# Optimization experiments

Measured on AMD Instinct MI355X. Metric: run time of the kernel, lower is better.

The kernel has to match this reference:

```python
import jax, jax.numpy as jnp
import numpy as np
from jax import ops as jops

N_NODES = 50000
N_EDGES = 800000
IN_CH = 128
HIDDEN = 32
HEADS = 8
OUT_CH = 128
NUM_GRAPHS = 64


def setup_inputs() -> dict:
    key = jax.random.key(0)
    ks = jax.random.split(key, 12)
    x = jax.random.normal(ks[0], (N_NODES, IN_CH), dtype=jnp.float32)
    edge_index = jax.random.randint(ks[1], (2, N_EDGES), 0, N_NODES, dtype=jnp.int64)
    batch = jnp.sort(jax.random.randint(ks[2], (N_NODES,), 0, NUM_GRAPHS, dtype=jnp.int64))
    HC = HEADS * HIDDEN  # 256
    s = lambda fan: 1.0 / np.sqrt(fan)
    W_gat = jax.random.normal(ks[3], (IN_CH, HC), dtype=jnp.float32) * s(IN_CH)
    att_src = jax.random.normal(ks[4], (HEADS, HIDDEN), dtype=jnp.float32) * s(HIDDEN)
    att_dst = jax.random.normal(ks[5], (HEADS, HIDDEN), dtype=jnp.float32) * s(HIDDEN)
    b_gat = jnp.zeros((HC,), dtype=jnp.float32)
    W1 = jax.random.normal(ks[6], (HC, HIDDEN), dtype=jnp.float32) * s(HC)
    b1 = jnp.zeros((HIDDEN,), dtype=jnp.float32)
    W2 = jax.random.normal(ks[7], (HIDDEN, HIDDEN), dtype=jnp.float32) * s(HIDDEN)
    b2 = jnp.zeros((HIDDEN,), dtype=jnp.float32)
    Wf = jax.random.normal(ks[8], (HIDDEN, OUT_CH), dtype=jnp.float32) * s(HIDDEN)
    bf = jnp.zeros((OUT_CH,), dtype=jnp.float32)
    return {"x": x, "edge_index": edge_index, "batch": batch,
            "W_gat": W_gat, "att_src": att_src, "att_dst": att_dst, "b_gat": b_gat,
            "W1": W1, "b1": b1, "W2": W2, "b2": b2, "Wf": Wf, "bf": bf}


def _gat(x, src, dst, N, W_gat, att_src, att_dst, b_gat):
    # h: [N, H, C]
    h = (x @ W_gat).reshape(N, HEADS, HIDDEN)
    a_s = jnp.sum(h * att_src[None], axis=-1)  # [N, H]
    a_d = jnp.sum(h * att_dst[None], axis=-1)  # [N, H]
    e = jax.nn.leaky_relu(a_s[src] + a_d[dst], negative_slope=0.2)  # [E, H]
    # per-destination-node softmax over incoming edges
    m = jops.segment_max(e, dst, num_segments=N)          # [N, H]
    ex = jnp.exp(e - m[dst])                              # [E, H]
    denom = jops.segment_sum(ex, dst, num_segments=N)     # [N, H]
    alpha = ex / denom[dst]                               # [E, H]
    msg = alpha[:, :, None] * h[src]                      # [E, H, C]
    out = jops.segment_sum(msg, dst, num_segments=N)      # [N, H, C]
    return out.reshape(N, HEADS * HIDDEN) + b_gat


def reference(x, edge_index, batch, W_gat, att_src, att_dst, b_gat,
              W1, b1, W2, b2, Wf, bf):
    N = x.shape[0]
    # GATConv (PyG default add_self_loops=True)
    loops = jnp.arange(N, dtype=edge_index.dtype)
    src = jnp.concatenate([edge_index[0], loops])
    dst = jnp.concatenate([edge_index[1], loops])
    out = jax.nn.relu(_gat(x, src, dst, N, W_gat, att_src, att_dst, b_gat))
    # GINConv (eps=0, no self-loops): nn((1+eps)*x + sum_{j->i} x_j)
    agg = jops.segment_sum(out[edge_index[0]], edge_index[1], num_segments=N)
    z = out + agg
    z = jax.nn.relu(z @ W1 + b1) @ W2 + b2
    z = jax.nn.relu(z)
    # global mean pool over graphs
    sums = jops.segment_sum(z, batch, num_segments=NUM_GRAPHS)
    counts = jops.segment_sum(jnp.ones((N,), dtype=z.dtype), batch, num_segments=NUM_GRAPHS)
    pooled = sums / jnp.maximum(counts, 1.0)[:, None]
    return pooled @ Wf + bf
```

## Files before the change

kernel.cpp:

```cpp
#include <hip/hip_runtime.h>

#define N_NODES 50000
#define N_EDGES 800000
#define HEADS   8
#define HID     32
#define HC      256
#define NG      64
#define GEMM_TILES (N_NODES / 16)
#define NBUCK   196
#define EBUF_CAP 5120
#define BUCKA_BLOCKS 196

typedef unsigned short ushort_t;
typedef unsigned int   uint_t;
typedef __attribute__((ext_vector_type(8))) short short8;
typedef __attribute__((ext_vector_type(4))) float f32x4;

#define HB_OFF    0
#define Z_OFF     0
#define AS_OFF    6400000
#define AD_OFF    6800000
#define ROW_OFF   7200000
#define BCNT_OFF  7250016
#define BBASE_OFF 7256288
#define GS_OFF    7256544
#define WGBT_OFF  7256640
#define W1BT_OFF  7273024
#define CSR_OFF   7277120
#define EBUF_OFF  8077120
#define Y_OFF     10084160
#define WS_END    10884160

__device__ __forceinline__ ushort_t f2bf(float f) {
    uint_t u = __float_as_uint(f);
    u = (u + 0x7FFFu + ((u >> 16) & 1u)) >> 16;
    return (ushort_t)u;
}
__device__ __forceinline__ float bf2f(ushort_t u) { return __uint_as_float((uint_t)u << 16); }
__device__ __forceinline__ float bf_lo(uint_t u) { return __uint_as_float(u << 16); }
__device__ __forceinline__ float bf_hi(uint_t u) { return __uint_as_float(u & 0xFFFF0000u); }

__global__ __launch_bounds__(256) void k_init(const float* __restrict__ Wg,
                                              const float* __restrict__ W1,
                                              ushort_t* __restrict__ wgbT,
                                              ushort_t* __restrict__ w1bT,
                                              float* __restrict__ bcntf) {
    int id = blockIdx.x * 256 + threadIdx.x;
    if (id < 32768) {
        wgbT[(id & 255) * 128 + (id >> 8)] = f2bf(Wg[id]);
    } else if (id < 32768 + 1568) {
        ((float4*)bcntf)[id - 32768] = make_float4(0.f, 0.f, 0.f, 0.f);
    } else if (id < 32768 + 1568 + 8192) {
        int j = id - 32768 - 1568;
        w1bT[(j & 31) * 256 + (j >> 5)] = f2bf(W1[j]);
    }
}

__global__ __launch_bounds__(256) void k_gemm_bucketA(const float* __restrict__ x,
                                                      const ushort_t* __restrict__ wgbT,
                                                      const float* __restrict__ att_s,
                                                      const float* __restrict__ att_d,
                                                      ushort_t* __restrict__ hb,
                                                      float* __restrict__ a_s,
                                                      float* __restrict__ a_d,
                                                      const int* __restrict__ batch,
                                                      int* __restrict__ gs,
                                                      const int* __restrict__ ei,
                                                      int* __restrict__ bcnt,
                                                      int* __restrict__ ebuf) {
    if (blockIdx.x < BUCKA_BLOCKS) {
        __shared__ int h[NBUCK];
        __shared__ int base[NBUCK];
        int kb = blockIdx.x;
        int t = threadIdx.x;
        if (t < NBUCK) h[t] = 0;
        __syncthreads();
        int pack[16];
#pragma unroll
        for (int i = 0; i < 16; ++i) {
            int e = kb * 4096 + i * 256 + t;
            pack[i] = -1;
            if (e < N_EDGES) {
                int b = ei[N_EDGES + e] >> 8;
                int lp = atomicAdd(&h[b], 1);
                pack[i] = (b << 16) | lp;
            }
        }
        __syncthreads();
        if (t < NBUCK && h[t] > 0) base[t] = atomicAdd(&bcnt[t * 32], h[t]);
        __syncthreads();
        int2* eb = (int2*)ebuf;
#pragma unroll
        for (int i = 0; i < 16; ++i) {
            if (pack[i] >= 0) {
                int e = kb * 4096 + i * 256 + t;
                int b = pack[i] >> 16, lp = pack[i] & 0xFFFF;
                eb[(size_t)b * EBUF_CAP + base[b] + lp] = make_int2(ei[e], ei[N_EDGES + e]);
            }
        }
        return;
    }

    int tile = blockIdx.x - BUCKA_BLOCKS;
    int w = threadIdx.x >> 6;
    int colbase = w * 64;
    int lane = threadIdx.x & 63;
    int n0 = tile * 16;
    int col = lane & 15, quad = lane >> 4;

    f32x4 acc[4];
#pragma unroll
    for (int i = 0; i < 4; ++i) acc[i] = (f32x4){0.f, 0.f, 0.f, 0.f};

    const float* xr = x + (size_t)(n0 + col) * 128 + quad * 8;
    const ushort_t* wbase = wgbT + (size_t)(colbase + col) * 128 + quad * 8;
#pragma unroll
    for (int kk = 0; kk < 4; ++kk) {
        float4 xa = *(const float4*)(xr + kk * 32);
        float4 xb = *(const float4*)(xr + kk * 32 + 4);
        short8 af;
        af[0] = (short)f2bf(xa.x); af[1] = (short)f2bf(xa.y);
        af[2] = (short)f2bf(xa.z); af[3] = (short)f2bf(xa.w);
        af[4] = (short)f2bf(xb.x); af[5] = (short)f2bf(xb.y);
        af[6] = (short)f2bf(xb.z); af[7] = (short)f2bf(xb.w);
#pragma unroll
        for (int nt = 0; nt < 4; ++nt) {
            short8 wf = *(const short8*)(wbase + nt * 16 * 128 + kk * 32);
            acc[nt] = __builtin_amdgcn_mfma_f32_16x16x32_bf16(wf, af, acc[nt], 0, 0, 0);
        }
    }

    int node = n0 + col;
    ushort_t* hrow = hb + (size_t)node * 256 + colbase + quad * 4;
#pragma unroll
    for (int nt = 0; nt < 4; ++nt) {
        uint2 o;
        o.x = (uint_t)f2bf(acc[nt][0]) | ((uint_t)f2bf(acc[nt][1]) << 16);
        o.y = (uint_t)f2bf(acc[nt][2]) | ((uint_t)f2bf(acc[nt][3]) << 16);
        *(uint2*)(hrow + nt * 16) = o;
    }

#pragma unroll
    for (int hl = 0; hl < 2; ++hl) {
        int hg = (colbase >> 5) + hl;
        float4 s0 = *(const float4*)(att_s + colbase + hl * 32 + quad * 4);
        float4 s1 = *(const float4*)(att_s + colbase + hl * 32 + 16 + quad * 4);
        float4 d0 = *(const float4*)(att_d + colbase + hl * 32 + quad * 4);
        float4 d1 = *(const float4*)(att_d + colbase + hl * 32 + 16 + quad * 4);
        f32x4 e = acc[2 * hl], f = acc[2 * hl + 1];
        float ps = e[0]*s0.x + e[1]*s0.y + e[2]*s0.z + e[3]*s0.w
                 + f[0]*s1.x + f[1]*s1.y + f[2]*s1.z + f[3]*s1.w;
        float pd = e[0]*d0.x + e[1]*d0.y + e[2]*d0.z + e[3]*d0.w
                 + f[0]*d1.x + f[1]*d1.y + f[2]*d1.z + f[3]*d1.w;
        ps += __shfl_xor(ps, 16, 64); ps += __shfl_xor(ps, 32, 64);
        pd += __shfl_xor(pd, 16, 64); pd += __shfl_xor(pd, 32, 64);
        if (quad == 0) {
            a_s[(size_t)node * 8 + hg] = ps;
            a_d[(size_t)node * 8 + hg] = pd;
        }
    }

    int t = threadIdx.x;
    if (t < 16) {
        int n = n0 + t;
        int b0 = batch[n];
        int bp = (n == 0) ? -1 : batch[n - 1];
        for (int g2 = bp + 1; g2 <= b0; ++g2) gs[g2] = n;
        if (n == N_NODES - 1)
            for (int g2 = b0 + 1; g2 <= NG; ++g2) gs[g2] = N_NODES;
    }
}

__global__ __launch_bounds__(512) void k_bucketB(const int* __restrict__ ebuf,
                                                 const int* __restrict__ bcnt,
                                                 int* __restrict__ row,
                                                 int* __restrict__ csr) {
    __shared__ int h[256], sc[256], cur[256];
    int k = blockIdx.x, t = threadIdx.x;
    if (t < 256) sc[t] = (t < NBUCK) ? bcnt[t * 32] : 0;
    __syncthreads();
    for (int off = 1; off < 256; off <<= 1) {
        int u = 0;
        if (t < 256 && t >= off) u = sc[t - off];
        __syncthreads();
        if (t < 256) sc[t] += u;
        __syncthreads();
    }
    int base = (k == 0) ? 0 : sc[k - 1];
    int cnt = bcnt[k * 32];
    __syncthreads();
    if (t < 256) { h[t] = 0; cur[t] = 0; }
    __syncthreads();
    const int2* eb = (const int2*)ebuf + (size_t)k * EBUF_CAP;
    for (int i = t; i < cnt; i += 512) atomicAdd(&h[eb[i].y & 255], 1);
    __syncthreads();
    int v = (t < 256) ? h[t] : 0;
    if (t < 256) sc[t] = v;
    __syncthreads();
    for (int off = 1; off < 256; off <<= 1) {
        int u = 0;
        if (t < 256 && t >= off) u = sc[t - off];
        __syncthreads();
        if (t < 256) sc[t] += u;
        __syncthreads();
    }
    int lrow = 0;
    if (t < 256) {
        lrow = sc[t] - v;
        int n = k * 256 + t;
        if (n < N_NODES) row[n] = base + lrow;
    }
    if (k == 0 && t == 0) row[N_NODES] = N_EDGES;
    __syncthreads();
    if (t < 256) sc[t] = lrow;
    __syncthreads();
    for (int i = t; i < cnt; i += 512) {
        int2 sd = eb[i];
        int dl = sd.y & 255;
        int p = atomicAdd(&cur[dl], 1);
        csr[base + sc[dl] + p] = sd.x;
    }
}

__global__ __launch_bounds__(256) void k_gat_y(const int* __restrict__ row,
                                               const int* __restrict__ csr,
                                               const float* __restrict__ a_s,
                                               const float* __restrict__ a_d,
                                               const ushort_t* __restrict__ hb,
                                               const float* __restrict__ bg,
                                               const ushort_t* __restrict__ w1bT,
                                               ushort_t* __restrict__ yb) {
    __shared__ ushort_t s_out[16][264];
    int w = threadIdx.x >> 6;
    int lane = threadIdx.x & 63;
    int n0 = blockIdx.x * 16;

    int c    = lane & 31;
    int half = lane >> 5;
    int hd   = c >> 2;
    const char* as_hd = (const char*)(a_s + hd);
    const char* hlane = (const char*)hb + c * 16;
    float4 b0 = *(const float4*)(bg + c * 8);
    float4 b1 = *(const float4*)(bg + c * 8 + 4);

    for (int i = 0; i < 4; ++i) {
        int n = n0 + w * 4 + i;
        int r0 = row[n], r1 = row[n + 1];
        int deg = r1 - r0;
        float ad2 = a_d[n * 8 + hd];
        const int* cp = csr + r0;

        float acc[8];
        float psum;
        {
            float vs = *(const float*)(as_hd + ((size_t)n << 5)) + ad2;
            vs = vs > 0.f ? vs : 0.2f * vs;
            float evs = __expf(vs);
            float wq = (half == 0) ? evs : 0.f;
            uint4 su = *(const uint4*)(hlane + ((size_t)n << 9));
            acc[0] = wq * bf_lo(su.x); acc[1] = wq * bf_hi(su.x);
            acc[2] = wq * bf_lo(su.y); acc[3] = wq * bf_hi(su.y);
            acc[4] = wq * bf_lo(su.z); acc[5] = wq * bf_hi(su.z);
            acc[6] = wq * bf_lo(su.w); acc[7] = wq * bf_hi(su.w);
            psum = wq;
        }

        int j = half;
        for (; j + 6 < deg; j += 8) {
            int   sx[4];
            float av[4];
            uint4 uu[4];
#pragma unroll
            for (int q = 0; q < 4; ++q) sx[q] = cp[j + 2 * q];
#pragma unroll
            for (int q = 0; q < 4; ++q) av[q] = *(const float*)(as_hd + ((size_t)sx[q] << 5));
#pragma unroll
            for (int q = 0; q < 4; ++q) uu[q] = *(const uint4*)(hlane + ((size_t)sx[q] << 9));
#pragma unroll
            for (int q = 0; q < 4; ++q) {
                float v = av[q] + ad2;
                v = v > 0.f ? v : 0.2f * v;
                float ev = __expf(v);
                psum += ev;
                acc[0] = fmaf(ev, bf_lo(uu[q].x), acc[0]);
                acc[1] = fmaf(ev, bf_hi(uu[q].x), acc[1]);
                acc[2] = fmaf(ev, bf_lo(uu[q].y), acc[2]);
                acc[3] = fmaf(ev, bf_hi(uu[q].y), acc[3]);
                acc[4] = fmaf(ev, bf_lo(uu[q].z), acc[4]);
                acc[5] = fmaf(ev, bf_hi(uu[q].z), acc[5]);
                acc[6] = fmaf(ev, bf_lo(uu[q].w), acc[6]);
                acc[7] = fmaf(ev, bf_hi(uu[q].w), acc[7]);
            }
        }
        for (; j < deg; j += 2) {
            int sj = cp[j];
            float v = *(const float*)(as_hd + ((size_t)sj << 5)) + ad2;
            v = v > 0.f ? v : 0.2f * v;
            float ev = __expf(v);
            psum += ev;
            uint4 u = *(const uint4*)(hlane + ((size_t)sj << 9));
            acc[0] = fmaf(ev, bf_lo(u.x), acc[0]);
            acc[1] = fmaf(ev, bf_hi(u.x), acc[1]);
            acc[2] = fmaf(ev, bf_lo(u.y), acc[2]);
            acc[3] = fmaf(ev, bf_hi(u.y), acc[3]);
            acc[4] = fmaf(ev, bf_lo(u.z), acc[4]);
            acc[5] = fmaf(ev, bf_hi(u.z), acc[5]);
            acc[6] = fmaf(ev, bf_lo(u.w), acc[6]);
            acc[7] = fmaf(ev, bf_hi(u.w), acc[7]);
        }

        psum += __shfl_xor(psum, 32, 64);
#pragma unroll
        for (int k2 = 0; k2 < 8; ++k2) acc[k2] += __shfl_xor(acc[k2], 32, 64);

        float inv = 1.0f / psum;
        float o0 = fmaxf(fmaf(acc[0], inv, b0.x), 0.f);
        float o1 = fmaxf(fmaf(acc[1], inv, b0.y), 0.f);
        float o2 = fmaxf(fmaf(acc[2], inv, b0.z), 0.f);
        float o3 = fmaxf(fmaf(acc[3], inv, b0.w), 0.f);
        float o4 = fmaxf(fmaf(acc[4], inv, b1.x), 0.f);
        float o5 = fmaxf(fmaf(acc[5], inv, b1.y), 0.f);
        float o6 = fmaxf(fmaf(acc[6], inv, b1.z), 0.f);
        float o7 = fmaxf(fmaf(acc[7], inv, b1.w), 0.f);
        uint4 o;
        o.x = (uint_t)f2bf(o0) | ((uint_t)f2bf(o1) << 16);
        o.y = (uint_t)f2bf(o2) | ((uint_t)f2bf(o3) << 16);
        o.z = (uint_t)f2bf(o4) | ((uint_t)f2bf(o5) << 16);
        o.w = (uint_t)f2bf(o6) | ((uint_t)f2bf(o7) << 16);
        if (half == 0)
            *(uint4*)&s_out[w * 4 + i][c * 8] = o;
    }
    __syncthreads();

    if (w < 2) {
        int col = lane & 15, quad = lane >> 4;
        f32x4 acc = (f32x4){0.f, 0.f, 0.f, 0.f};
        const ushort_t* ar = &s_out[col][quad * 8];
        const ushort_t* bp = w1bT + (w * 16 + col) * 256 + quad * 8;
#pragma unroll
        for (int kk = 0; kk < 8; ++kk) {
            short8 af = *(const short8*)(ar + kk * 32);
            short8 bf0 = *(const short8*)(bp + kk * 32);
            acc = __builtin_amdgcn_mfma_f32_16x16x32_bf16(af, bf0, acc, 0, 0, 0);
        }
        ushort_t* yr = yb + (size_t)(n0 + quad * 4) * 32 + w * 16 + col;
#pragma unroll
        for (int r = 0; r < 4; ++r)
            yr[r * 32] = f2bf(acc[r]);
    }
}

__global__ __launch_bounds__(256) void k_gin_mlp(const int* __restrict__ row,
                                                 const int* __restrict__ csr,
                                                 const ushort_t* __restrict__ yb,
                                                 const float* __restrict__ b1,
                                                 const float* __restrict__ W2,
                                                 const float* __restrict__ b2,
                                                 float* __restrict__ z) {
    __shared__ float s_z[4][32];
    int g = threadIdx.x >> 6;
    int lane = threadIdx.x & 63;
    int n = blockIdx.x * 4 + g;
    int col = lane & 31, half = lane >> 5;
    int r0 = row[n], r1 = row[n + 1];
    const char* ycol = (const char*)(yb + col);
    float acc = (half == 0) ? (bf2f(yb[(size_t)n * 32 + col]) + b1[col]) : 0.f;
    int j = r0 + half;
    for (; j + 14 < r1; j += 16) {
        int ss[8];
#pragma unroll
        for (int i = 0; i < 8; ++i) ss[i] = csr[j + 2 * i];
        float vv[8];
#pragma unroll
        for (int i = 0; i < 8; ++i)
            vv[i] = bf2f(*(const ushort_t*)(ycol + ((size_t)ss[i] << 6)));
        acc += ((vv[0] + vv[1]) + (vv[2] + vv[3])) + ((vv[4] + vv[5]) + (vv[6] + vv[7]));
    }
    for (; j + 6 < r1; j += 8) {
        int s0 = csr[j], s1 = csr[j + 2], s2 = csr[j + 4], s3 = csr[j + 6];
        float v0 = bf2f(*(const ushort_t*)(ycol + ((size_t)s0 << 6)));
        float v1 = bf2f(*(const ushort_t*)(ycol + ((size_t)s1 << 6)));
        float v2 = bf2f(*(const ushort_t*)(ycol + ((size_t)s2 << 6)));
        float v3 = bf2f(*(const ushort_t*)(ycol + ((size_t)s3 << 6)));
        acc += (v0 + v1) + (v2 + v3);
    }
    for (; j < r1; j += 2)
        acc += bf2f(*(const ushort_t*)(ycol + ((size_t)csr[j] << 6)));
    acc += __shfl_xor(acc, 32, 64);
    float z1 = fmaxf(acc, 0.f);
    if (lane < 32) s_z[g][col] = z1;
    const float* zr = &s_z[g][0];
    int k0 = half * 16;
    float p = 0.f;
#pragma unroll
    for (int k = 0; k < 16; k += 4) {
        float4 zv = *(const float4*)(zr + k0 + k);
        p = fmaf(zv.x, W2[(k0 + k + 0) * 32 + col], p);
        p = fmaf(zv.y, W2[(k0 + k + 1) * 32 + col], p);
        p = fmaf(zv.z, W2[(k0 + k + 2) * 32 + col], p);
        p = fmaf(zv.w, W2[(k0 + k + 3) * 32 + col], p);
    }
    p += __shfl_xor(p, 32, 64);
    if (lane < 32) z[n * 32 + col] = fmaxf(p + b2[col], 0.f);
}

__global__ __launch_bounds__(128) void k_pool_final(const float* __restrict__ z,
                                                    const int* __restrict__ gs,
                                                    const float* __restrict__ Wf,
                                                    const float* __restrict__ bf,
                                                    float* __restrict__ outp) {
    __shared__ float part[4][32];
    __shared__ float sums[32];
    int g = blockIdx.x;
    int t = threadIdx.x;
    int col = t & 31, q = t >> 5;
    int r0 = gs[g], r1 = gs[g + 1];
    float s = 0.f;
    for (int r = r0 + q; r < r1; r += 4) s += z[r * 32 + col];
    part[q][col] = s;
    __syncthreads();
    if (t < 32) sums[t] = part[0][t] + part[1][t] + part[2][t] + part[3][t];
    __syncthreads();
    float inv = 1.0f / fmaxf((float)(r1 - r0), 1.0f);
    float acc = 0.f;
#pragma unroll
    for (int k = 0; k < 32; ++k)
        acc = fmaf(sums[k], Wf[k * 128 + t], acc);
    outp[g * 128 + t] = acc * inv + bf[t];
}

extern "C" void kernel_launch(void* const* d_in, const int* in_sizes, int n_in,
                              void* d_out, int out_size, void* d_ws, size_t ws_size,
                              hipStream_t stream) {
    const float* x     = (const float*)d_in[0];
    const int*   ei    = (const int*)d_in[1];
    const int*   batch = (const int*)d_in[2];
    const float* Wg    = (const float*)d_in[3];
    const float* att_s = (const float*)d_in[4];
    const float* att_d = (const float*)d_in[5];
    const float* bg    = (const float*)d_in[6];
    const float* W1    = (const float*)d_in[7];
    const float* b1    = (const float*)d_in[8];
    const float* W2    = (const float*)d_in[9];
    const float* b2    = (const float*)d_in[10];
    const float* Wf    = (const float*)d_in[11];
    const float* bf    = (const float*)d_in[12];
    float* ws = (float*)d_ws;

    ushort_t* hb   = (ushort_t*)(ws + HB_OFF);
    float* z       = ws + Z_OFF;
    float* a_s     = ws + AS_OFF;
    float* a_d     = ws + AD_OFF;
    int*   row     = (int*)(ws + ROW_OFF);
    int*   bcnt    = (int*)(ws + BCNT_OFF);
    int*   gs      = (int*)(ws + GS_OFF);
    ushort_t* wgbT = (ushort_t*)(ws + WGBT_OFF);
    ushort_t* w1bT = (ushort_t*)(ws + W1BT_OFF);
    int*   csr     = (int*)(ws + CSR_OFF);
    int*   ebuf    = (int*)(ws + EBUF_OFF);
    ushort_t* yb   = (ushort_t*)(ws + Y_OFF);

    k_init<<<(32768 + 1568 + 8192 + 255) / 256, 256, 0, stream>>>(Wg, W1, wgbT, w1bT, (float*)bcnt);

    k_gemm_bucketA<<<BUCKA_BLOCKS + GEMM_TILES, 256, 0, stream>>>(
        x, wgbT, att_s, att_d, hb, a_s, a_d, batch, gs, ei, bcnt, ebuf);

    k_bucketB<<<NBUCK, 512, 0, stream>>>(ebuf, bcnt, row, csr);

    k_gat_y<<<N_NODES / 16, 256, 0, stream>>>(row, csr, a_s, a_d, hb, bg, w1bT, yb);

    k_gin_mlp<<<N_NODES / 4, 256, 0, stream>>>(row, csr, yb, b1, W2, b2, z);

    k_pool_final<<<NG, 128, 0, stream>>>(z, gs, Wf, bf, (float*)d_out);
}
```

Before: 301.8 us.

## Regroup pipeline kernels: fuse weight init with bucketA, bucketB with GAT GEMM

Measured after the change: 309.7 us. 1.03x slower.

```diff
diff --git a/kernel.cpp b/kernel.cpp
--- a/kernel.cpp
+++ b/kernel.cpp
@@ -10,6 +10,7 @@
 #define NBUCK   196
 #define EBUF_CAP 5120
 #define BUCKA_BLOCKS 196
+#define INIT_BLOCKS 160
 
 typedef unsigned short ushort_t;
 typedef unsigned int   uint_t;
@@ -40,23 +41,59 @@
 __device__ __forceinline__ float bf_lo(uint_t u) { return __uint_as_float(u << 16); }
 __device__ __forceinline__ float bf_hi(uint_t u) { return __uint_as_float(u & 0xFFFF0000u); }
 
-__global__ __launch_bounds__(256) void k_init(const float* __restrict__ Wg,
-                                              const float* __restrict__ W1,
-                                              ushort_t* __restrict__ wgbT,
-                                              ushort_t* __restrict__ w1bT,
-                                              float* __restrict__ bcntf) {
-    int id = blockIdx.x * 256 + threadIdx.x;
-    if (id < 32768) {
-        wgbT[(id & 255) * 128 + (id >> 8)] = f2bf(Wg[id]);
-    } else if (id < 32768 + 1568) {
-        ((float4*)bcntf)[id - 32768] = make_float4(0.f, 0.f, 0.f, 0.f);
-    } else if (id < 32768 + 1568 + 8192) {
-        int j = id - 32768 - 1568;
-        w1bT[(j & 31) * 256 + (j >> 5)] = f2bf(W1[j]);
-    }
-}
-
-__global__ __launch_bounds__(256) void k_gemm_bucketA(const float* __restrict__ x,
+__global__ __launch_bounds__(256) void k_init_bucketA(const float* __restrict__ Wg,
+                                                      const float* __restrict__ W1,
+                                                      ushort_t* __restrict__ wgbT,
+                                                      ushort_t* __restrict__ w1bT,
+                                                      const int* __restrict__ ei,
+                                                      int* __restrict__ bcnt,
+                                                      int* __restrict__ ebuf) {
+    if (blockIdx.x < INIT_BLOCKS) {
+        int id = blockIdx.x * 256 + threadIdx.x;
+        if (id < 32768) {
+            wgbT[(id & 255) * 128 + (id >> 8)] = f2bf(Wg[id]);
+        } else {
+            int j = id - 32768;
+            w1bT[(j & 31) * 256 + (j >> 5)] = f2bf(W1[j]);
+        }
+        return;
+    }
+    __shared__ int h[NBUCK];
+    __shared__ int base[NBUCK];
+    int kb = blockIdx.x - INIT_BLOCKS;
+    int t = threadIdx.x;
+    if (t < NBUCK) h[t] = 0;
+    __syncthreads();
+    int pack[16];
+#pragma unroll
+    for (int i = 0; i < 16; ++i) {
+        int e = kb * 4096 + i * 256 + t;
+        pack[i] = -1;
+        if (e < N_EDGES) {
+            int b = ei[N_EDGES + e] >> 8;
+            int lp = atomicAdd(&h[b], 1);
+            pack[i] = (b << 16) | lp;
+        }
+    }
+    __syncthreads();
+    if (t < NBUCK && h[t] > 0) base[t] = atomicAdd(&bcnt[t * 32], h[t]);
+    __syncthreads();
+    int2* eb = (int2*)ebuf;
+#pragma unroll
+    for (int i = 0; i < 16; ++i) {
+        if (pack[i] >= 0) {
+            int e = kb * 4096 + i * 256 + t;
+            int b = pack[i] >> 16, lp = pack[i] & 0xFFFF;
+            eb[(size_t)b * EBUF_CAP + base[b] + lp] = make_int2(ei[e], ei[N_EDGES + e]);
+        }
+    }
+}
+
+__global__ __launch_bounds__(256) void k_bucketB_gemm(const int* __restrict__ ebuf,
+                                                      const int* __restrict__ bcnt,
+                                                      int* __restrict__ row,
+                                                      int* __restrict__ csr,
+                                                      const float* __restrict__ x,
                                                       const ushort_t* __restrict__ wgbT,
                                                       const float* __restrict__ att_s,
                                                       const float* __restrict__ att_d,
@@ -64,44 +101,52 @@
                                                       float* __restrict__ a_s,
                                                       float* __restrict__ a_d,
                                                       const int* __restrict__ batch,
-                                                      int* __restrict__ gs,
-                                                      const int* __restrict__ ei,
-                                                      int* __restrict__ bcnt,
-                                                      int* __restrict__ ebuf) {
-    if (blockIdx.x < BUCKA_BLOCKS) {
-        __shared__ int h[NBUCK];
-        __shared__ int base[NBUCK];
-        int kb = blockIdx.x;
-        int t = threadIdx.x;
-        if (t < NBUCK) h[t] = 0;
-        __syncthreads();
-        int pack[16];
-#pragma unroll
-        for (int i = 0; i < 16; ++i) {
-            int e = kb * 4096 + i * 256 + t;
-            pack[i] = -1;
-            if (e < N_EDGES) {
-                int b = ei[N_EDGES + e] >> 8;
-                int lp = atomicAdd(&h[b], 1);
-                pack[i] = (b << 16) | lp;
-            }
-        }
-        __syncthreads();
-        if (t < NBUCK && h[t] > 0) base[t] = atomicAdd(&bcnt[t * 32], h[t]);
-        __syncthreads();
-        int2* eb = (int2*)ebuf;
-#pragma unroll
-        for (int i = 0; i < 16; ++i) {
-            if (pack[i] >= 0) {
-                int e = kb * 4096 + i * 256 + t;
-                int b = pack[i] >> 16, lp = pack[i] & 0xFFFF;
-                eb[(size_t)b * EBUF_CAP + base[b] + lp] = make_int2(ei[e], ei[N_EDGES + e]);
-            }
+                                                      int* __restrict__ gs) {
+    if (blockIdx.x < NBUCK) {
+        __shared__ int h[256], sc[256], cur[256];
+        int k = blockIdx.x, t = threadIdx.x;
+        sc[t] = (t < NBUCK) ? bcnt[t * 32] : 0;
+        __syncthreads();
+        for (int off = 1; off < 256; off <<= 1) {
+            int u = (t >= off) ? sc[t - off] : 0;
+            __syncthreads();
+            sc[t] += u;
+            __syncthreads();
+        }
+        int base = (k == 0) ? 0 : sc[k - 1];
+        int cnt = bcnt[k * 32];
+        __syncthreads();
+        h[t] = 0; cur[t] = 0;
+        __syncthreads();
+        const int2* eb = (const int2*)ebuf + (size_t)k * EBUF_CAP;
+        for (int i = t; i < cnt; i += 256) atomicAdd(&h[eb[i].y & 255], 1);
+        __syncthreads();
+        int v = h[t];
+        sc[t] = v;
+        __syncthreads();
+        for (int off = 1; off < 256; off <<= 1) {
+            int u = (t >= off) ? sc[t - off] : 0;
+            __syncthreads();
+            sc[t] += u;
+            __syncthreads();
+        }
+        int lrow = sc[t] - v;
+        int n = k * 256 + t;
+        if (n < N_NODES) row[n] = base + lrow;
+        if (k == 0 && t == 0) row[N_NODES] = N_EDGES;
+        __syncthreads();
+        sc[t] = lrow;
+        __syncthreads();
+        for (int i = t; i < cnt; i += 256) {
+            int2 sd = eb[i];
+            int dl = sd.y & 255;
+            int p = atomicAdd(&cur[dl], 1);
+            csr[base + sc[dl] + p] = sd.x;
         }
         return;
     }
 
-    int tile = blockIdx.x - BUCKA_BLOCKS;
+    int tile = blockIdx.x - NBUCK;
     int w = threadIdx.x >> 6;
     int colbase = w * 64;
     int lane = threadIdx.x & 63;
@@ -171,57 +216,6 @@
     }
 }
 
-__global__ __launch_bounds__(512) void k_bucketB(const int* __restrict__ ebuf,
-                                                 const int* __restrict__ bcnt,
-                                                 int* __restrict__ row,
-                                                 int* __restrict__ csr) {
-    __shared__ int h[256], sc[256], cur[256];
-    int k = blockIdx.x, t = threadIdx.x;
-    if (t < 256) sc[t] = (t < NBUCK) ? bcnt[t * 32] : 0;
-    __syncthreads();
-    for (int off = 1; off < 256; off <<= 1) {
-        int u = 0;
-        if (t < 256 && t >= off) u = sc[t - off];
-        __syncthreads();
-        if (t < 256) sc[t] += u;
-        __syncthreads();
-    }
-    int base = (k == 0) ? 0 : sc[k - 1];
-    int cnt = bcnt[k * 32];
-    __syncthreads();
-    if (t < 256) { h[t] = 0; cur[t] = 0; }
-    __syncthreads();
-    const int2* eb = (const int2*)ebuf + (size_t)k * EBUF_CAP;
-    for (int i = t; i < cnt; i += 512) atomicAdd(&h[eb[i].y & 255], 1);
-    __syncthreads();
-    int v = (t < 256) ? h[t] : 0;
-    if (t < 256) sc[t] = v;
-    __syncthreads();
-    for (int off = 1; off < 256; off <<= 1) {
-        int u = 0;
-        if (t < 256 && t >= off) u = sc[t - off];
-        __syncthreads();
-        if (t < 256) sc[t] += u;
-        __syncthreads();
-    }
-    int lrow = 0;
-    if (t < 256) {
-        lrow = sc[t] - v;
-        int n = k * 256 + t;
-        if (n < N_NODES) row[n] = base + lrow;
-    }
-    if (k == 0 && t == 0) row[N_NODES] = N_EDGES;
-    __syncthreads();
-    if (t < 256) sc[t] = lrow;
-    __syncthreads();
-    for (int i = t; i < cnt; i += 512) {
-        int2 sd = eb[i];
-        int dl = sd.y & 255;
-        int p = atomicAdd(&cur[dl], 1);
-        csr[base + sc[dl] + p] = sd.x;
-    }
-}
-
 __global__ __launch_bounds__(256) void k_gat_y(const int* __restrict__ row,
                                                const int* __restrict__ csr,
                                                const float* __restrict__ a_s,
@@ -266,6 +260,32 @@
         }
 
         int j = half;
+        for (; j + 14 < deg; j += 16) {
+            int   sx[8];
+            float av[8];
+            uint4 uu[8];
+#pragma unroll
+            for (int q = 0; q < 8; ++q) sx[q] = cp[j + 2 * q];
+#pragma unroll
+            for (int q = 0; q < 8; ++q) av[q] = *(const float*)(as_hd + ((size_t)sx[q] << 5));
+#pragma unroll
+            for (int q = 0; q < 8; ++q) uu[q] = *(const uint4*)(hlane + ((size_t)sx[q] << 9));
+#pragma unroll
+            for (int q = 0; q < 8; ++q) {
+                float v = av[q] + ad2;
+                v = v > 0.f ? v : 0.2f * v;
+                float ev = __expf(v);
+                psum += ev;
+                acc[0] = fmaf(ev, bf_lo(uu[q].x), acc[0]);
+                acc[1] = fmaf(ev, bf_hi(uu[q].x), acc[1]);
+                acc[2] = fmaf(ev, bf_lo(uu[q].y), acc[2]);
+                acc[3] = fmaf(ev, bf_hi(uu[q].y), acc[3]);
+                acc[4] = fmaf(ev, bf_lo(uu[q].z), acc[4]);
+                acc[5] = fmaf(ev, bf_hi(uu[q].z), acc[5]);
+                acc[6] = fmaf(ev, bf_lo(uu[q].w), acc[6]);
+                acc[7] = fmaf(ev, bf_hi(uu[q].w), acc[7]);
+            }
+        }
         for (; j + 6 < deg; j += 8) {
             int   sx[4];
             float av[4];
@@ -460,12 +480,13 @@
     int*   ebuf    = (int*)(ws + EBUF_OFF);
     ushort_t* yb   = (ushort_t*)(ws + Y_OFF);
 
-    k_init<<<(32768 + 1568 + 8192 + 255) / 256, 256, 0, stream>>>(Wg, W1, wgbT, w1bT, (float*)bcnt);
-
-    k_gemm_bucketA<<<BUCKA_BLOCKS + GEMM_TILES, 256, 0, stream>>>(
-        x, wgbT, att_s, att_d, hb, a_s, a_d, batch, gs, ei, bcnt, ebuf);
-
-    k_bucketB<<<NBUCK, 512, 0, stream>>>(ebuf, bcnt, row, csr);
+    hipMemsetAsync(bcnt, 0, NBUCK * 32 * sizeof(int), stream);
+
+    k_init_bucketA<<<INIT_BLOCKS + BUCKA_BLOCKS, 256, 0, stream>>>(
+        Wg, W1, wgbT, w1bT, ei, bcnt, ebuf);
+
+    k_bucketB_gemm<<<NBUCK + GEMM_TILES, 256, 0, stream>>>(
+        ebuf, bcnt, row, csr, x, wgbT, att_s, att_d, hb, a_s, a_d, batch, gs);
 
     k_gat_y<<<N_NODES / 16, 256, 0, stream>>>(row, csr, a_s, a_d, hb, bg, w1bT, yb);
 
```
